# Optimization experiments

Measured on AMD Instinct MI355X. Metric: run time of the kernel, lower is better.

Reference implementation:

```python
import jax, jax.numpy as jnp
import numpy as np

N, IN_F, OUT_F = 8192, 512, 256
ALPHA = 0.2  # LeakyReLU negative slope
NEG_INF = -9e15


def setup_inputs() -> dict:
    key = jax.random.key(0)
    k1, k2, k3, k4 = jax.random.split(key, 4)
    input = jax.random.normal(k1, (N, IN_F), dtype=jnp.float32)
    adj = jax.random.randint(k2, (N, N), 0, 2, dtype=jnp.int32)
    # Xavier-like scale for params
    W = jax.random.normal(k3, (IN_F, OUT_F), dtype=jnp.float32) * (1.414 * np.sqrt(2.0 / (IN_F + OUT_F)))
    a = jax.random.normal(k4, (2 * OUT_F, 1), dtype=jnp.float32) * (1.414 * np.sqrt(2.0 / (2 * OUT_F + 1)))
    return {"input": input, "adj": adj, "W": W, "a": a}


def reference(input, adj, W, a):
    h = input @ W                                   # [N, F]
    a1, a2 = a[:OUT_F, 0], a[OUT_F:, 0]             # [F], [F]
    # e[i, j] = leakyrelu(h_i . a1 + h_j . a2) -- equivalent to concat+linear
    s1 = h @ a1                                     # [N]
    s2 = h @ a2                                     # [N]
    e = jax.nn.leaky_relu(s1[:, None] + s2[None, :], negative_slope=ALPHA)  # [N, N]
    e = jnp.where(adj > 0, e, NEG_INF)
    attention = jax.nn.softmax(e, axis=1)           # row-wise softmax
    # dropout p=0.0 / eval mode -> identity
    h_prime = attention @ h                          # [N, F]
    return jax.nn.elu(h_prime)                       # concat=True -> elu
```

## Files before the change

kernel.cpp:

```cpp
#include <hip/hip_runtime.h>
#include <stdint.h>

#define N_NODES 8192
#define IN_FEAT 512
#define OUT_FEAT 256
#define LOG2E 1.4426950408889634f

typedef __bf16 b16x8 __attribute__((ext_vector_type(8)));
typedef unsigned short u16x8v __attribute__((ext_vector_type(8)));
typedef float f32x4 __attribute__((ext_vector_type(4)));
typedef float f32x16 __attribute__((ext_vector_type(16)));

static __device__ __forceinline__ unsigned short f2bf(float f) {
    union { float f; uint32_t u; } v; v.f = f;
    uint32_t r = v.u + 0x7FFFu + ((v.u >> 16) & 1u);
    return (unsigned short)(r >> 16);
}

__global__ __launch_bounds__(256) void k_pack(const int* __restrict__ adj,
                                              unsigned char* __restrict__ bitsR,
                                              const float* __restrict__ W,
                                              unsigned short* __restrict__ Wt) {
    size_t t = (size_t)blockIdx.x * 256 + threadIdx.x;
    const int4* a4 = (const int4*)adj + t * 2;
    int4 x0 = a4[0];
    int4 x1 = a4[1];
    unsigned b = (unsigned)(x0.x != 0)
               | ((unsigned)(x0.y != 0) << 1)
               | ((unsigned)(x0.z != 0) << 2)
               | ((unsigned)(x0.w != 0) << 3)
               | ((unsigned)(x1.x != 0) << 4)
               | ((unsigned)(x1.y != 0) << 5)
               | ((unsigned)(x1.z != 0) << 6)
               | ((unsigned)(x1.w != 0) << 7);
    bitsR[t] = (unsigned char)b;
    if (blockIdx.x < 512) {
        int t0 = blockIdx.x * 256 + threadIdx.x;
        int c = t0 & (OUT_FEAT - 1);
        int k = t0 >> 8;
        Wt[(size_t)c * IN_FEAT + k] = f2bf(W[(size_t)k * OUT_FEAT + c]);
    }
}

__global__ __launch_bounds__(256) void k1_hgemm(const float* __restrict__ input,
                                                const unsigned short* __restrict__ Wt,
                                                const float* __restrict__ a_vec,
                                                unsigned short* __restrict__ hTf32,
                                                float* __restrict__ s1_raw,
                                                float* __restrict__ s2_raw) {
    int tid = threadIdx.x;
    int lane = tid & 63;
    int c = lane & 15, g = lane >> 4;
    int r0 = blockIdx.x * 64 + (tid >> 6) * 16;
    f32x4 acc[16];
#pragma unroll
    for (int t = 0; t < 16; ++t) acc[t] = (f32x4){0.f, 0.f, 0.f, 0.f};
    const float* arow = input + (size_t)(r0 + c) * IN_FEAT;
#pragma unroll 1
    for (int kk = 0; kk < IN_FEAT / 32; ++kk) {
        int kb = kk * 32 + 8 * g;
        float4 x0 = *(const float4*)(arow + kb);
        float4 x1 = *(const float4*)(arow + kb + 4);
        u16x8v au;
        au[0] = f2bf(x0.x); au[1] = f2bf(x0.y); au[2] = f2bf(x0.z); au[3] = f2bf(x0.w);
        au[4] = f2bf(x1.x); au[5] = f2bf(x1.y); au[6] = f2bf(x1.z); au[7] = f2bf(x1.w);
        b16x8 af = __builtin_bit_cast(b16x8, au);
#pragma unroll
        for (int t = 0; t < 16; ++t) {
            b16x8 bf = __builtin_bit_cast(b16x8,
                *(const u16x8v*)(Wt + (size_t)(16 * t + c) * IN_FEAT + kb));
            acc[t] = __builtin_amdgcn_mfma_f32_16x16x32_bf16(af, bf, acc[t], 0, 0, 0);
        }
    }
    float a1v[16], a2v[16];
#pragma unroll
    for (int t = 0; t < 16; ++t) {
        a1v[t] = a_vec[16 * t + c];
        a2v[t] = a_vec[OUT_FEAT + 16 * t + c];
    }
#pragma unroll
    for (int r = 0; r < 4; ++r) {
        float s1p = 0.f, s2p = 0.f;
#pragma unroll
        for (int t = 0; t < 16; ++t) { s1p += acc[t][r] * a1v[t]; s2p += acc[t][r] * a2v[t]; }
#pragma unroll
        for (int m = 1; m <= 8; m <<= 1) { s1p += __shfl_xor(s1p, m); s2p += __shfl_xor(s2p, m); }
        if (c == 0) {
            int row = r0 + 4 * g + r;
            s1_raw[row] = s1p;
            s2_raw[row] = s2p;
        }
    }
    int chunk16 = r0 >> 4;
    int lane_base = c + 32 * (g >> 1);
    int e0 = 4 * (g & 1);
#pragma unroll
    for (int t = 0; t < 16; ++t) {
        ushort4 pk;
        pk.x = f2bf(acc[t][0]); pk.y = f2bf(acc[t][1]);
        pk.z = f2bf(acc[t][2]); pk.w = f2bf(acc[t][3]);
        int lane_t = 16 * (t & 1) + lane_base;
        *(ushort4*)(hTf32 + ((size_t)(chunk16 * 8 + (t >> 1)) * 64 + lane_t) * 8 + e0) = pk;
    }
}

__global__ __launch_bounds__(256) void k2_prep(const float* __restrict__ s1_raw,
                                               const float* __restrict__ s2_raw,
                                               float* __restrict__ e12,
                                               float2* __restrict__ row2) {
    __shared__ float red[256];
    int tid = threadIdx.x;
    float m = -3.0e38f;
    for (int j = tid; j < N_NODES; j += 256) m = fmaxf(m, s2_raw[j]);
    red[tid] = m;
    __syncthreads();
    for (int s = 128; s > 0; s >>= 1) {
        if (tid < s) red[tid] = fmaxf(red[tid], red[tid + s]);
        __syncthreads();
    }
    float M2 = red[0];
    int i = blockIdx.x * 256 + tid;
    float s1 = s1_raw[i];
    float u = s1 + M2;
    float mi = fmaxf(u, 0.2f * u);
    row2[i] = make_float2(__builtin_amdgcn_exp2f((s1 - mi) * LOG2E),
                          __builtin_amdgcn_exp2f((0.2f * s1 - mi) * LOG2E));
    float s2 = s2_raw[i];
    e12[2 * i]     = __builtin_amdgcn_exp2f(s2 * LOG2E);
    e12[2 * i + 1] = __builtin_amdgcn_exp2f(0.2f * s2 * LOG2E);
}

__global__ __launch_bounds__(256, 4) void k3_flash(const uint32_t* __restrict__ maskR,
                                                   const unsigned short* __restrict__ hTf32,
                                                   const float* __restrict__ e12g,
                                                   const float2* __restrict__ row2,
                                                   float* __restrict__ pout,
                                                   float* __restrict__ rowpart) {
    __shared__ __align__(16) float le12[4096];
    __shared__ __align__(16) unsigned short laf[8][512];
    __shared__ float lsum[4][64];

    int tid = threadIdx.x;
    int cq = tid >> 6, lane = tid & 63;
    int lr = lane & 31, lo = lane >> 5;
    int jq = blockIdx.x & 3;
    int rg = blockIdx.x >> 2;
    int rowbase = rg * 32;

#pragma unroll
    for (int q = 0; q < 4; ++q) {
        *(float4*)&le12[tid * 16 + q * 4] =
            *(const float4*)(e12g + (size_t)jq * 4096 + tid * 16 + q * 4);
    }
    float2 rc = row2[rowbase + lr];
    float E1r = rc.x, E2r = rc.y;
    __syncthreads();

    const int4* m4 = (const int4*)(maskR + (size_t)(rowbase + lr) * 256 + jq * 64);

    f32x16 acc0 = {0}, acc1 = {0};
    float lacc = 0.f;
    int4 mq = m4[0];

#pragma unroll 1
    for (int kc8 = 0; kc8 < 16; ++kc8) {
        uint32_t md[4] = {(uint32_t)mq.x, (uint32_t)mq.y, (uint32_t)mq.z, (uint32_t)mq.w};

#pragma unroll
        for (int hh = 0; hh < 2; ++hh) {
            int sl = hh * 4 + cq;
            int kc = kc8 * 8 + sl;
            float ev[16];
#pragma unroll
            for (int q = 0; q < 4; ++q)
                *(f32x4*)&ev[q * 4] = *(const f32x4*)&le12[(kc * 16 + 8 * lo) * 2 + q * 4];
            uint32_t mb = (md[sl >> 1] >> (16 * (sl & 1) + 8 * lo)) & 0xFFu;
            b16x8 af;
#pragma unroll
            for (int e = 0; e < 8; ++e) {
                float q0 = fmaxf(E1r * ev[2 * e], E2r * ev[2 * e + 1]);
                float p = (mb & (1u << e)) ? q0 : 0.f;
                lacc += p;
                af[e] = (__bf16)p;
            }
            *(u16x8v*)&laf[sl][lane * 8] = __builtin_bit_cast(u16x8v, af);
        }
        __syncthreads();

        if (kc8 < 15) mq = m4[kc8 + 1];

        int gchunk0 = jq * 128 + kc8 * 8;
#pragma unroll
        for (int s = 0; s < 8; ++s) {
            const unsigned short* tb =
                hTf32 + ((size_t)((gchunk0 + s) * 8 + 2 * cq) * 64 + lane) * 8;
            b16x8 bf0 = __builtin_bit_cast(b16x8, *(const u16x8v*)(tb));
            b16x8 bf1 = __builtin_bit_cast(b16x8, *(const u16x8v*)(tb + 512));
            b16x8 afs = __builtin_bit_cast(b16x8, *(const u16x8v*)&laf[s][lane * 8]);
            acc0 = __builtin_amdgcn_mfma_f32_32x32x16_bf16(afs, bf0, acc0, 0, 0, 0);
            acc1 = __builtin_amdgcn_mfma_f32_32x32x16_bf16(afs, bf1, acc1, 0, 0, 0);
        }
        __syncthreads();
    }

    lsum[cq][lane] = lacc;
    __syncthreads();
    if (cq == 0) {
        float l = lsum[0][lane] + lsum[1][lane] + lsum[2][lane] + lsum[3][lane];
        float ltot = l + __shfl_xor(l, 32);
        if (lo == 0) rowpart[jq * N_NODES + rowbase + lr] = ltot;
    }

#pragma unroll
    for (int reg = 0; reg < 16; ++reg) {
        int row = (reg & 3) + 8 * (reg >> 2) + 4 * lo;
        size_t base = ((size_t)jq * N_NODES + rowbase + row) * OUT_FEAT + cq * 64 + lr;
        pout[base] = acc0[reg];
        pout[base + 32] = acc1[reg];
    }
}

__global__ __launch_bounds__(256) void k4_reduce(const float* __restrict__ pout,
                                                 const float* __restrict__ rowpart,
                                                 float* __restrict__ out) {
    int t = blockIdx.x * 256 + threadIdx.x;
    int row = t >> 8;
    float s = 0.f, l = 0.f;
#pragma unroll
    for (int q = 0; q < 4; ++q) {
        s += pout[(size_t)q * N_NODES * OUT_FEAT + t];
        l += rowpart[q * N_NODES + row];
    }
    float inv = (l > 0.f) ? 1.0f / l : 0.f;
    float x = s * inv;
    out[t] = (x > 0.f) ? x : (__builtin_amdgcn_exp2f(x * LOG2E) - 1.0f);
}

extern "C" void kernel_launch(void* const* d_in, const int* in_sizes, int n_in,
                              void* d_out, int out_size, void* d_ws, size_t ws_size,
                              hipStream_t stream) {
    const float* input = (const float*)d_in[0];
    const int* adj = (const int*)d_in[1];
    const float* W = (const float*)d_in[2];
    const float* a_vec = (const float*)d_in[3];
    float* out = (float*)d_out;

    char* ws = (char*)d_ws;
    unsigned short* Wt    = (unsigned short*)(ws);
    unsigned short* hTf32 = (unsigned short*)(ws + 262144);
    float*  e12     = (float*)(ws + 4456448);
    float2* row2    = (float2*)(ws + 4521984);
    float*  s1_raw  = (float*)(ws + 4587520);
    float*  s2_raw  = (float*)(ws + 4620288);
    unsigned char* bitsR = (unsigned char*)(ws + 4653056);
    float*  rowpart = (float*)(ws + 13041664);
    float*  pout    = (float*)(ws + 13172736);

    hipLaunchKernelGGL(k_pack, dim3(32768), dim3(256), 0, stream, adj, bitsR, W, Wt);
    hipLaunchKernelGGL(k1_hgemm, dim3(N_NODES / 64), dim3(256), 0, stream,
                       input, Wt, a_vec, hTf32, s1_raw, s2_raw);
    hipLaunchKernelGGL(k2_prep, dim3(32), dim3(256), 0, stream, s1_raw, s2_raw, e12, row2);
    hipLaunchKernelGGL(k3_flash, dim3(1024), dim3(256), 0, stream,
                       (const uint32_t*)bitsR, hTf32, e12, row2, pout, rowpart);
    hipLaunchKernelGGL(k4_reduce, dim3(N_NODES * OUT_FEAT / 256), dim3(256), 0, stream,
                       pout, rowpart, out);
}
```

Before: 157.8 us.

## Double-buffer attention-probability LDS tile to overlap production with MFMA

The shared-memory tile of bf16 attention probabilities is double-buffered. The next chunk's masked exponentials are computed into the alternate buffer while MFMAs consume the current one, which removes one barrier per iteration. The aim is to overlap the VALU probability generation with matrix-core work and global h loads. The cost is 8KB more LDS per block, which may reduce occupancy under the 4-blocks-per-CU launch bound, plus a prologue step.

```diff
diff --git a/kernel.cpp b/kernel.cpp
--- a/kernel.cpp
+++ b/kernel.cpp
@@ -137,7 +137,7 @@
                                                    float* __restrict__ pout,
                                                    float* __restrict__ rowpart) {
     __shared__ __align__(16) float le12[4096];
-    __shared__ __align__(16) unsigned short laf[8][512];
+    __shared__ __align__(16) unsigned short laf[2][8][512];
     __shared__ float lsum[4][64];
 
     int tid = threadIdx.x;
@@ -160,34 +160,47 @@
 
     f32x16 acc0 = {0}, acc1 = {0};
     float lacc = 0.f;
-    int4 mq = m4[0];
+
+#define PRODUCE_GROUP(BUF, KC8, MD)                                                      \
+    {                                                                                    \
+        _Pragma("unroll")                                                                \
+        for (int hh = 0; hh < 2; ++hh) {                                                 \
+            int sl = hh * 4 + cq;                                                        \
+            int kc = (KC8) * 8 + sl;                                                     \
+            float ev[16];                                                                \
+            _Pragma("unroll")                                                            \
+            for (int q = 0; q < 4; ++q)                                                  \
+                *(f32x4*)&ev[q * 4] = *(const f32x4*)&le12[(kc * 16 + 8 * lo) * 2 + q * 4]; \
+            uint32_t mb = ((MD)[sl >> 1] >> (16 * (sl & 1) + 8 * lo)) & 0xFFu;           \
+            b16x8 af;                                                                    \
+            _Pragma("unroll")                                                            \
+            for (int e = 0; e < 8; ++e) {                                                \
+                float q0 = fmaxf(E1r * ev[2 * e], E2r * ev[2 * e + 1]);                  \
+                float p = (mb & (1u << e)) ? q0 : 0.f;                                   \
+                lacc += p;                                                               \
+                af[e] = (__bf16)p;                                                       \
+            }                                                                            \
+            *(u16x8v*)&laf[BUF][sl][lane * 8] = __builtin_bit_cast(u16x8v, af);          \
+        }                                                                                \
+    }
+
+    {
+        int4 mq0 = m4[0];
+        uint32_t md[4] = {(uint32_t)mq0.x, (uint32_t)mq0.y, (uint32_t)mq0.z, (uint32_t)mq0.w};
+        PRODUCE_GROUP(0, 0, md)
+    }
+    int4 mq = m4[1];
+    __syncthreads();
 
 #pragma unroll 1
     for (int kc8 = 0; kc8 < 16; ++kc8) {
-        uint32_t md[4] = {(uint32_t)mq.x, (uint32_t)mq.y, (uint32_t)mq.z, (uint32_t)mq.w};
-
-#pragma unroll
-        for (int hh = 0; hh < 2; ++hh) {
-            int sl = hh * 4 + cq;
-            int kc = kc8 * 8 + sl;
-            float ev[16];
-#pragma unroll
-            for (int q = 0; q < 4; ++q)
-                *(f32x4*)&ev[q * 4] = *(const f32x4*)&le12[(kc * 16 + 8 * lo) * 2 + q * 4];
-            uint32_t mb = (md[sl >> 1] >> (16 * (sl & 1) + 8 * lo)) & 0xFFu;
-            b16x8 af;
-#pragma unroll
-            for (int e = 0; e < 8; ++e) {
-                float q0 = fmaxf(E1r * ev[2 * e], E2r * ev[2 * e + 1]);
-                float p = (mb & (1u << e)) ? q0 : 0.f;
-                lacc += p;
-                af[e] = (__bf16)p;
-            }
-            *(u16x8v*)&laf[sl][lane * 8] = __builtin_bit_cast(u16x8v, af);
-        }
-        __syncthreads();
-
-        if (kc8 < 15) mq = m4[kc8 + 1];
+        int cur = kc8 & 1;
+
+        if (kc8 < 15) {
+            uint32_t md[4] = {(uint32_t)mq.x, (uint32_t)mq.y, (uint32_t)mq.z, (uint32_t)mq.w};
+            PRODUCE_GROUP(cur ^ 1, kc8 + 1, md)
+            if (kc8 < 14) mq = m4[kc8 + 2];
+        }
 
         int gchunk0 = jq * 128 + kc8 * 8;
 #pragma unroll
@@ -196,12 +209,13 @@
                 hTf32 + ((size_t)((gchunk0 + s) * 8 + 2 * cq) * 64 + lane) * 8;
             b16x8 bf0 = __builtin_bit_cast(b16x8, *(const u16x8v*)(tb));
             b16x8 bf1 = __builtin_bit_cast(b16x8, *(const u16x8v*)(tb + 512));
-            b16x8 afs = __builtin_bit_cast(b16x8, *(const u16x8v*)&laf[s][lane * 8]);
+            b16x8 afs = __builtin_bit_cast(b16x8, *(const u16x8v*)&laf[cur][s][lane * 8]);
             acc0 = __builtin_amdgcn_mfma_f32_32x32x16_bf16(afs, bf0, acc0, 0, 0, 0);
             acc1 = __builtin_amdgcn_mfma_f32_32x32x16_bf16(afs, bf1, acc1, 0, 0, 0);
         }
         __syncthreads();
     }
+#undef PRODUCE_GROUP
 
     lsum[cq][lane] = lacc;
     __syncthreads();
```

After: 158.1 us. No clear change (+0.2%).

## Fuse adjacency bit-packing into flash kernel, split j into 8 chunks, bf16 partials

Applied to the files above, without the earlier changes.

The separate adjacency packing pass is removed. Each flash block now reads its 32x1024 slice of the int32 adjacency directly, packs it to bits in shared memory and consumes it from there, so the packed mask no longer goes to global memory and back. The column dimension is split eight ways instead of four, doubling the grid, and the partial outputs are stored as bf16 to halve partial-sum traffic into the reduce kernel. The cost is more partial buffers to reduce and some extra rounding error from bf16 partials.

```diff
diff --git a/kernel.cpp b/kernel.cpp
--- a/kernel.cpp
+++ b/kernel.cpp
@@ -16,30 +16,17 @@
     uint32_t r = v.u + 0x7FFFu + ((v.u >> 16) & 1u);
     return (unsigned short)(r >> 16);
 }
-
-__global__ __launch_bounds__(256) void k_pack(const int* __restrict__ adj,
-                                              unsigned char* __restrict__ bitsR,
-                                              const float* __restrict__ W,
-                                              unsigned short* __restrict__ Wt) {
-    size_t t = (size_t)blockIdx.x * 256 + threadIdx.x;
-    const int4* a4 = (const int4*)adj + t * 2;
-    int4 x0 = a4[0];
-    int4 x1 = a4[1];
-    unsigned b = (unsigned)(x0.x != 0)
-               | ((unsigned)(x0.y != 0) << 1)
-               | ((unsigned)(x0.z != 0) << 2)
-               | ((unsigned)(x0.w != 0) << 3)
-               | ((unsigned)(x1.x != 0) << 4)
-               | ((unsigned)(x1.y != 0) << 5)
-               | ((unsigned)(x1.z != 0) << 6)
-               | ((unsigned)(x1.w != 0) << 7);
-    bitsR[t] = (unsigned char)b;
-    if (blockIdx.x < 512) {
-        int t0 = blockIdx.x * 256 + threadIdx.x;
-        int c = t0 & (OUT_FEAT - 1);
-        int k = t0 >> 8;
-        Wt[(size_t)c * IN_FEAT + k] = f2bf(W[(size_t)k * OUT_FEAT + c]);
-    }
+static __device__ __forceinline__ float bf2f(unsigned short s) {
+    union { uint32_t u; float f; } v; v.u = ((uint32_t)s) << 16;
+    return v.f;
+}
+
+__global__ __launch_bounds__(256) void k0_transpose_w(const float* __restrict__ W,
+                                                      unsigned short* __restrict__ Wt) {
+    int tid = blockIdx.x * 256 + threadIdx.x;
+    int c = tid & (OUT_FEAT - 1);
+    int k = tid >> 8;
+    Wt[(size_t)c * IN_FEAT + k] = f2bf(W[(size_t)k * OUT_FEAT + c]);
 }
 
 __global__ __launch_bounds__(256) void k1_hgemm(const float* __restrict__ input,
@@ -130,40 +117,52 @@
     e12[2 * i + 1] = __builtin_amdgcn_exp2f(0.2f * s2 * LOG2E);
 }
 
-__global__ __launch_bounds__(256, 4) void k3_flash(const uint32_t* __restrict__ maskR,
+__global__ __launch_bounds__(256, 4) void k3_flash(const int* __restrict__ adj,
                                                    const unsigned short* __restrict__ hTf32,
                                                    const float* __restrict__ e12g,
                                                    const float2* __restrict__ row2,
-                                                   float* __restrict__ pout,
+                                                   unsigned short* __restrict__ poutb,
                                                    float* __restrict__ rowpart) {
-    __shared__ __align__(16) float le12[4096];
+    __shared__ __align__(16) float le12[2048];
     __shared__ __align__(16) unsigned short laf[8][512];
+    __shared__ __align__(16) uint32_t lmask[32 * 36];
     __shared__ float lsum[4][64];
 
     int tid = threadIdx.x;
     int cq = tid >> 6, lane = tid & 63;
     int lr = lane & 31, lo = lane >> 5;
-    int jq = blockIdx.x & 3;
-    int rg = blockIdx.x >> 2;
+    int jq = blockIdx.x & 7;
+    int rg = blockIdx.x >> 3;
     int rowbase = rg * 32;
 
-#pragma unroll
-    for (int q = 0; q < 4; ++q) {
-        *(float4*)&le12[tid * 16 + q * 4] =
-            *(const float4*)(e12g + (size_t)jq * 4096 + tid * 16 + q * 4);
+    *(float4*)&le12[tid * 8]     = *(const float4*)(e12g + (size_t)jq * 2048 + tid * 8);
+    *(float4*)&le12[tid * 8 + 4] = *(const float4*)(e12g + (size_t)jq * 2048 + tid * 8 + 4);
+
+#pragma unroll 4
+    for (int it = 0; it < 16; ++it) {
+        int b = it * 256 + tid;
+        int row = b >> 7;
+        int bir = b & 127;
+        const int4* src = (const int4*)(adj + (size_t)(rowbase + row) * N_NODES
+                                        + jq * 1024 + bir * 8);
+        int4 v0 = src[0];
+        int4 v1 = src[1];
+        unsigned pb = (unsigned)(v0.x != 0) | ((unsigned)(v0.y != 0) << 1)
+                    | ((unsigned)(v0.z != 0) << 2) | ((unsigned)(v0.w != 0) << 3)
+                    | ((unsigned)(v1.x != 0) << 4) | ((unsigned)(v1.y != 0) << 5)
+                    | ((unsigned)(v1.z != 0) << 6) | ((unsigned)(v1.w != 0) << 7);
+        ((unsigned char*)lmask)[row * 144 + bir] = (unsigned char)pb;
     }
     float2 rc = row2[rowbase + lr];
     float E1r = rc.x, E2r = rc.y;
     __syncthreads();
 
-    const int4* m4 = (const int4*)(maskR + (size_t)(rowbase + lr) * 256 + jq * 64);
-
     f32x16 acc0 = {0}, acc1 = {0};
     float lacc = 0.f;
-    int4 mq = m4[0];
 
 #pragma unroll 1
-    for (int kc8 = 0; kc8 < 16; ++kc8) {
+    for (int kc8 = 0; kc8 < 8; ++kc8) {
+        int4 mq = *(const int4*)((const char*)lmask + lr * 144 + kc8 * 16);
         uint32_t md[4] = {(uint32_t)mq.x, (uint32_t)mq.y, (uint32_t)mq.z, (uint32_t)mq.w};
 
 #pragma unroll
@@ -187,9 +186,7 @@
         }
         __syncthreads();
 
-        if (kc8 < 15) mq = m4[kc8 + 1];
-
-        int gchunk0 = jq * 128 + kc8 * 8;
+        int gchunk0 = jq * 64 + kc8 * 8;
 #pragma unroll
         for (int s = 0; s < 8; ++s) {
             const unsigned short* tb =
@@ -215,20 +212,20 @@
     for (int reg = 0; reg < 16; ++reg) {
         int row = (reg & 3) + 8 * (reg >> 2) + 4 * lo;
         size_t base = ((size_t)jq * N_NODES + rowbase + row) * OUT_FEAT + cq * 64 + lr;
-        pout[base] = acc0[reg];
-        pout[base + 32] = acc1[reg];
-    }
-}
-
-__global__ __launch_bounds__(256) void k4_reduce(const float* __restrict__ pout,
+        poutb[base] = f2bf(acc0[reg]);
+        poutb[base + 32] = f2bf(acc1[reg]);
+    }
+}
+
+__global__ __launch_bounds__(256) void k4_reduce(const unsigned short* __restrict__ poutb,
                                                  const float* __restrict__ rowpart,
                                                  float* __restrict__ out) {
     int t = blockIdx.x * 256 + threadIdx.x;
     int row = t >> 8;
     float s = 0.f, l = 0.f;
 #pragma unroll
-    for (int q = 0; q < 4; ++q) {
-        s += pout[(size_t)q * N_NODES * OUT_FEAT + t];
+    for (int q = 0; q < 8; ++q) {
+        s += bf2f(poutb[(size_t)q * N_NODES * OUT_FEAT + t]);
         l += rowpart[q * N_NODES + row];
     }
     float inv = (l > 0.f) ? 1.0f / l : 0.f;
@@ -252,16 +249,15 @@
     float2* row2    = (float2*)(ws + 4521984);
     float*  s1_raw  = (float*)(ws + 4587520);
     float*  s2_raw  = (float*)(ws + 4620288);
-    unsigned char* bitsR = (unsigned char*)(ws + 4653056);
-    float*  rowpart = (float*)(ws + 13041664);
-    float*  pout    = (float*)(ws + 13172736);
-
-    hipLaunchKernelGGL(k_pack, dim3(32768), dim3(256), 0, stream, adj, bitsR, W, Wt);
+    float*  rowpart = (float*)(ws + 4653056);
+    unsigned short* poutb = (unsigned short*)(ws + 4915200);
+
+    hipLaunchKernelGGL(k0_transpose_w, dim3(512), dim3(256), 0, stream, W, Wt);
     hipLaunchKernelGGL(k1_hgemm, dim3(N_NODES / 64), dim3(256), 0, stream,
                        input, Wt, a_vec, hTf32, s1_raw, s2_raw);
     hipLaunchKernelGGL(k2_prep, dim3(32), dim3(256), 0, stream, s1_raw, s2_raw, e12, row2);
-    hipLaunchKernelGGL(k3_flash, dim3(1024), dim3(256), 0, stream,
-                       (const uint32_t*)bitsR, hTf32, e12, row2, pout, rowpart);
+    hipLaunchKernelGGL(k3_flash, dim3(2048), dim3(256), 0, stream,
+                       adj, hTf32, e12, row2, poutb, rowpart);
     hipLaunchKernelGGL(k4_reduce, dim3(N_NODES * OUT_FEAT / 256), dim3(256), 0, stream,
-                       pout, rowpart, out);
-}
+                       poutb, rowpart, out);
+}
```

After: 155.0 us. No clear change (-1.7%).
